# Optimization experiments

Hardware: AMD Instinct MI355X
Metric: run time of the kernel (lower is better)

## Reference

```python
import jax, jax.numpy as jnp
import numpy as np
from jax.ops import segment_sum, segment_max

N_ENT = 50000
N_REL = 200
E = 800000
D = 128      # entity_dim
R = 128      # relation_dim
H = 8        # num_heads
HD = D // H  # head_dim
SLOPE = 0.2  # LeakyReLU negative slope

def leaky(x):
    return jnp.where(x >= 0, x, SLOPE * x)

def setup_inputs() -> dict:
    key = jax.random.key(0)
    ks = jax.random.split(key, 8)
    h = jax.random.normal(ks[0], (N_ENT, D), dtype=jnp.float32)
    z = jax.random.normal(ks[1], (N_REL, R), dtype=jnp.float32)
    # weights stored (in_features, out_features); scaled ~ kaiming-ish
    Wc_w = jax.random.normal(ks[2], (D + R, D), dtype=jnp.float32) / np.sqrt(D + R)
    P_w = jax.random.normal(ks[3], (2 * D + R, D), dtype=jnp.float32) / np.sqrt(2 * D + R)
    y_w = jax.random.normal(ks[4], (D, H), dtype=jnp.float32) / np.sqrt(D)
    residual_weight = jnp.ones((1,), dtype=jnp.float32)
    edge_index = jax.random.randint(ks[5], (2, E), 0, N_ENT, dtype=jnp.int32)
    edge_type = jax.random.randint(ks[6], (E,), 0, N_REL, dtype=jnp.int32)
    return {"h": h, "z": z, "Wc_w": Wc_w, "P_w": P_w, "y_w": y_w,
            "residual_weight": residual_weight,
            "edge_index": edge_index, "edge_type": edge_type}

def reference(h, z, Wc_w, P_w, y_w, residual_weight, edge_index, edge_type):
    src, dst = edge_index[0], edge_index[1]
    n = h.shape[0]
    # per-destination degree and mean relation embedding z_bar_i
    deg = segment_sum(jnp.ones_like(dst, dtype=h.dtype), dst, num_segments=n)  # (N,)
    z_edge = z[edge_type]                                                      # (E,R)
    z_bar = segment_sum(z_edge, dst, num_segments=n) / jnp.maximum(deg, 1.0)[:, None]  # (N,R)
    # split P_hat over the concat [h_i || h_j || z_k]
    P1, P2, P3 = P_w[:D], P_w[D:2 * D], P_w[2 * D:]
    hP1 = h @ P1   # (N,D) dst part
    hP2 = h @ P2   # (N,D) src part
    zP3 = z @ P3   # (N_REL,D)
    pre_edge = hP1[dst] + hP2[src] + zP3[edge_type]      # (E,D)
    attn_e = leaky(pre_edge) @ y_w                        # (E,H)
    pre_self = hP1 + hP2 + z_bar @ P3                     # (N,D)  b_self=[h_i,h_i,z_bar]
    attn_s = leaky(pre_self) @ y_w                        # (N,H)
    # segment softmax over {self} U incoming edges, per head
    m_e = segment_max(attn_e, dst, num_segments=n)        # -inf for empty segments
    m = jnp.maximum(attn_s, m_e)                          # (N,H)
    e_e = jnp.exp(attn_e - m[dst])                        # (E,H)
    e_s = jnp.exp(attn_s - m)                             # (N,H)
    denom = segment_sum(e_e, dst, num_segments=n) + e_s   # (N,H)
    w_e = e_e / denom[dst]                                # (E,H)
    w_s = e_s / denom                                     # (N,H)
    # Wc over concats [h || z]
    Wc_h, Wc_z = Wc_w[:D], Wc_w[D:]
    hWc = h @ Wc_h                                        # (N,D)
    zWc = z @ Wc_z                                        # (N_REL,D)
    t_e = hWc[src] + zWc[edge_type]                       # (E,D)
    t_s = hWc + z_bar @ Wc_z                              # (N,D)
    # per-head weighted sum
    agg_e = segment_sum(w_e[:, :, None] * t_e.reshape(-1, H, HD), dst, num_segments=n)
    agg = agg_e + w_s[:, :, None] * t_s.reshape(-1, H, HD)  # (N,H,HD)
    h_new = leaky(agg.reshape(-1, D) + residual_weight * h)
    # nodes without incoming edges keep their original representation
    return jnp.where(deg[:, None] > 0, h_new, h)
```

## Files before the change

### kernel.cpp

```cpp
#include <hip/hip_runtime.h>

#define NE 50000
#define NR 200
#define EE 800000
#define DD 128
#define HH 8
#define SLOTS 64
#define SLOPE 0.2f

__device__ __forceinline__ float leaky(float x){ return x >= 0.f ? x : SLOPE*x; }

__device__ __forceinline__ float head_reduce(float4 pa, float4 pb, int hh){
  bool b0 = (hh & 1) != 0;
  bool b1 = (hh & 2) != 0;
  bool b2 = (hh & 4) != 0;
  float q0 = (b0 ? pa.y : pa.x) + __shfl_xor(b0 ? pa.x : pa.y, 1, 64);
  float q1 = (b0 ? pa.w : pa.z) + __shfl_xor(b0 ? pa.z : pa.w, 1, 64);
  float q2 = (b0 ? pb.y : pb.x) + __shfl_xor(b0 ? pb.x : pb.y, 1, 64);
  float q3 = (b0 ? pb.w : pb.z) + __shfl_xor(b0 ? pb.z : pb.w, 1, 64);
  float r0 = (b1 ? q1 : q0) + __shfl_xor(b1 ? q0 : q1, 2, 64);
  float r1 = (b1 ? q3 : q2) + __shfl_xor(b1 ? q2 : q3, 2, 64);
  float a  = (b2 ? r1 : r0) + __shfl_xor(b2 ? r0 : r1, 4, 64);
  a += __shfl_xor(a, 8, 64);
  a += __shfl_xor(a, 16, 64);
  a += __shfl_xor(a, 32, 64);
  return a;
}

__global__ void k_zero(int* __restrict__ cnt){
  int i = blockIdx.x*256 + threadIdx.x;
  if (i < NE) cnt[i] = 0;
}

__global__ void k_scatter(const int* __restrict__ edge_index,
                          const int* __restrict__ edge_type,
                          int* __restrict__ cnt, int* __restrict__ slot){
  int e = blockIdx.x*256 + threadIdx.x;
  if (e >= EE) return;
  int s = edge_index[e];
  int d = edge_index[EE + e];
  int t = edge_type[e];
  int pos = atomicAdd(&cnt[d], 1);
  if (pos < SLOTS) slot[d*SLOTS + pos] = s | (t << 16);
}

__global__ void k_zsmall(const float* __restrict__ z, const float* __restrict__ P_w,
                         const float* __restrict__ Wc_w,
                         float* __restrict__ zP3, float* __restrict__ zWc){
  int r = blockIdx.x, c = threadIdx.x;
  float a1 = 0.f, a2 = 0.f;
  for (int d = 0; d < DD; d++){
    float zv = z[r*DD + d];
    a1 = fmaf(zv, P_w[(2*DD + d)*DD + c], a1);
    a2 = fmaf(zv, Wc_w[(DD + d)*DD + c], a2);
  }
  zP3[r*DD + c] = a1;
  zWc[r*DD + c] = a2;
}

__global__ __launch_bounds__(256) void k_hgemm(const float* __restrict__ h,
    const float* __restrict__ P_w, const float* __restrict__ Wc_w,
    float* __restrict__ hP1, float* __restrict__ hP2, float* __restrict__ hWc){
  __shared__ float hs[64][DD + 4];
  int tid = threadIdx.x;
  int row0 = blockIdx.x * 64;
  for (int f = tid; f < 64*DD/4; f += 256){
    int r = f >> 5, c4 = f & 31;
    int gr = row0 + r;
    float4 v = (gr < NE) ? ((const float4*)(h + (size_t)gr*DD))[c4]
                         : make_float4(0.f,0.f,0.f,0.f);
    hs[r][c4*4+0] = v.x; hs[r][c4*4+1] = v.y;
    hs[r][c4*4+2] = v.z; hs[r][c4*4+3] = v.w;
  }
  __syncthreads();
  int r0 = (tid >> 4) * 4, c0 = (tid & 15) * 8;
  #pragma unroll
  for (int mi = 0; mi < 3; mi++){
    const float* W = (mi == 0) ? P_w : (mi == 1) ? (P_w + DD*DD) : Wc_w;
    float*       O = (mi == 0) ? hP1 : (mi == 1) ? hP2 : hWc;
    float acc[4][8];
    #pragma unroll
    for (int i = 0; i < 4; i++)
      #pragma unroll
      for (int j = 0; j < 8; j++) acc[i][j] = 0.f;
    for (int d = 0; d < DD; d++){
      float av[4];
      #pragma unroll
      for (int i = 0; i < 4; i++) av[i] = hs[r0+i][d];
      float4 b0 = *(const float4*)(W + d*DD + c0);
      float4 b1 = *(const float4*)(W + d*DD + c0 + 4);
      float bv[8] = {b0.x,b0.y,b0.z,b0.w,b1.x,b1.y,b1.z,b1.w};
      #pragma unroll
      for (int i = 0; i < 4; i++)
        #pragma unroll
        for (int j = 0; j < 8; j++)
          acc[i][j] = fmaf(av[i], bv[j], acc[i][j]);
    }
    #pragma unroll
    for (int i = 0; i < 4; i++){
      int gr = row0 + r0 + i;
      if (gr < NE){
        *(float4*)(O + (size_t)gr*DD + c0)     = make_float4(acc[i][0],acc[i][1],acc[i][2],acc[i][3]);
        *(float4*)(O + (size_t)gr*DD + c0 + 4) = make_float4(acc[i][4],acc[i][5],acc[i][6],acc[i][7]);
      }
    }
  }
}

__global__ __launch_bounds__(256) void k_node(
    const float* __restrict__ hP1, const float* __restrict__ hP2,
    const float* __restrict__ hWc, const float* __restrict__ zP3,
    const float* __restrict__ zWc, const float* __restrict__ h,
    const float* __restrict__ y_w, const float* __restrict__ rw_p,
    const int* __restrict__ cnt, const int* __restrict__ slot,
    float* __restrict__ out){
  int lane = threadIdx.x & 63;
  int n = blockIdx.x*4 + (threadIdx.x >> 6);
  if (n >= NE) return;
  int hh  = lane & 7;
  int sub = lane >> 3;
  int di  = hh*8 + sub;
  int deg = cnt[n]; if (deg > SLOTS) deg = SLOTS;
  float2 hn = ((const float2*)(h + (size_t)n*DD))[di];
  if (deg == 0){ ((float2*)(out + (size_t)n*DD))[di] = hn; return; }
  float2 p1  = ((const float2*)(hP1 + (size_t)n*DD))[di];
  float2 p2n = ((const float2*)(hP2 + (size_t)n*DD))[di];
  float2 wcn = ((const float2*)(hWc + (size_t)n*DD))[di];
  int d0 = di*2;
  const float4* y4 = (const float4*)(y_w + (size_t)d0*HH);
  float4 A = y4[0], B = y4[1], C = y4[2], Dv = y4[3];
  int my_slot = 0;
  if (lane < deg) my_slot = slot[(size_t)n*SLOTS + lane];
  float m_h = -1e30f, den = 0.f;
  float aggx = 0.f, aggy = 0.f;
  float sP3x = 0.f, sP3y = 0.f, sWcx = 0.f, sWcy = 0.f;
  for (int j = 0; j < deg; j++){
    int v = __shfl(my_slot, j, 64);
    int s = v & 0xFFFF;
    int t = v >> 16;
    float2 a2 = ((const float2*)(hP2 + (size_t)s*DD))[di];
    float2 b2 = ((const float2*)(zP3 + (size_t)t*DD))[di];
    float2 c2 = ((const float2*)(hWc + (size_t)s*DD))[di];
    float2 e2 = ((const float2*)(zWc + (size_t)t*DD))[di];
    sP3x += b2.x; sP3y += b2.y;
    sWcx += e2.x; sWcy += e2.y;
    float l0 = leaky(p1.x + a2.x + b2.x);
    float l1 = leaky(p1.y + a2.y + b2.y);
    float4 pa, pb;
    pa.x = l0*A.x + l1*C.x;  pa.y = l0*A.y + l1*C.y;
    pa.z = l0*A.z + l1*C.z;  pa.w = l0*A.w + l1*C.w;
    pb.x = l0*B.x + l1*Dv.x; pb.y = l0*B.y + l1*Dv.y;
    pb.z = l0*B.z + l1*Dv.z; pb.w = l0*B.w + l1*Dv.w;
    float attn = head_reduce(pa, pb, hh);
    float nm = fmaxf(m_h, attn);
    float sc = __expf(m_h - nm);
    float w  = __expf(attn - nm);
    den = den*sc + w;
    m_h = nm;
    float tx = c2.x + e2.x, ty = c2.y + e2.y;
    aggx = aggx*sc + w*tx;
    aggy = aggy*sc + w*ty;
  }
  float invdeg = 1.f/(float)deg;
  float l0 = leaky(p1.x + p2n.x + sP3x*invdeg);
  float l1 = leaky(p1.y + p2n.y + sP3y*invdeg);
  float4 pa, pb;
  pa.x = l0*A.x + l1*C.x;  pa.y = l0*A.y + l1*C.y;
  pa.z = l0*A.z + l1*C.z;  pa.w = l0*A.w + l1*C.w;
  pb.x = l0*B.x + l1*Dv.x; pb.y = l0*B.y + l1*Dv.y;
  pb.z = l0*B.z + l1*Dv.z; pb.w = l0*B.w + l1*Dv.w;
  float attnS = head_reduce(pa, pb, hh);
  float nm = fmaxf(m_h, attnS);
  float sc = __expf(m_h - nm);
  float w  = __expf(attnS - nm);
  den = den*sc + w;
  float tx = wcn.x + sWcx*invdeg, ty = wcn.y + sWcy*invdeg;
  aggx = aggx*sc + w*tx;
  aggy = aggy*sc + w*ty;
  float rw = rw_p[0];
  float inv_den = 1.f/den;
  float o0 = leaky(aggx*inv_den + rw*hn.x);
  float o1 = leaky(aggy*inv_den + rw*hn.y);
  ((float2*)(out + (size_t)n*DD))[di] = make_float2(o0, o1);
}

extern "C" void kernel_launch(void* const* d_in, const int* in_sizes, int n_in,
                              void* d_out, int out_size, void* d_ws, size_t ws_size,
                              hipStream_t stream){
  const float* h    = (const float*)d_in[0];
  const float* z    = (const float*)d_in[1];
  const float* Wc_w = (const float*)d_in[2];
  const float* P_w  = (const float*)d_in[3];
  const float* y_w  = (const float*)d_in[4];
  const float* rw   = (const float*)d_in[5];
  const int* edge_index = (const int*)d_in[6];
  const int* edge_type  = (const int*)d_in[7];
  float* out = (float*)d_out;

  char* ws = (char*)d_ws;
  float* hP1 = (float*)ws;  ws += (size_t)NE*DD*4;
  float* hP2 = (float*)ws;  ws += (size_t)NE*DD*4;
  float* hWc = (float*)ws;  ws += (size_t)NE*DD*4;
  float* zP3 = (float*)ws;  ws += (size_t)NR*DD*4;
  float* zWc = (float*)ws;  ws += (size_t)NR*DD*4;
  int*   cnt = (int*)ws;    ws += (size_t)NE*4;
  int*   slot= (int*)ws;    ws += (size_t)NE*SLOTS*4;

  hipLaunchKernelGGL(k_zero,    dim3((NE+255)/256), dim3(256), 0, stream, cnt);
  hipLaunchKernelGGL(k_scatter, dim3((EE+255)/256), dim3(256), 0, stream,
                     edge_index, edge_type, cnt, slot);
  hipLaunchKernelGGL(k_zsmall,  dim3(NR), dim3(DD), 0, stream, z, P_w, Wc_w, zP3, zWc);
  hipLaunchKernelGGL(k_hgemm,   dim3((NE+63)/64), dim3(256), 0, stream,
                     h, P_w, Wc_w, hP1, hP2, hWc);
  hipLaunchKernelGGL(k_node,    dim3((NE+3)/4), dim3(256), 0, stream,
                     hP1, hP2, hWc, zP3, zWc, h, y_w, rw, cnt, slot, out);
}
```

Measured before the change: 485.5 us.

## Interleave per-source projections and batch edge gathers four at a time

Stores hP2 and hWc interleaved in a single row (and zP3/zWc likewise), so each edge gather reads one contiguous 1KB row instead of two separate rows. The node kernel's edge loop is unrolled by four, issuing all gathers before the attention math to raise memory-level parallelism, and it uses readlane for the slot broadcast. The GEMM reads shared memory as float4 along the k dimension. The cost is more registers in the node kernel, which may reduce occupancy.

Measured after the change: 452.9 us. -6.7%, faster.

```diff
diff --git a/kernel.cpp b/kernel.cpp
--- a/kernel.cpp
+++ b/kernel.cpp
@@ -27,6 +27,29 @@
   return a;
 }
 
+__device__ __forceinline__ float edge_attn(float2 p1, float2 a, float2 b,
+    float4 A, float4 B, float4 C, float4 Dv, int hh){
+  float l0 = leaky(p1.x + a.x + b.x);
+  float l1 = leaky(p1.y + a.y + b.y);
+  float4 pa, pb;
+  pa.x = l0*A.x + l1*C.x;  pa.y = l0*A.y + l1*C.y;
+  pa.z = l0*A.z + l1*C.z;  pa.w = l0*A.w + l1*C.w;
+  pb.x = l0*B.x + l1*Dv.x; pb.y = l0*B.y + l1*Dv.y;
+  pb.z = l0*B.z + l1*Dv.z; pb.w = l0*B.w + l1*Dv.w;
+  return head_reduce(pa, pb, hh);
+}
+
+__device__ __forceinline__ void sm_update(float attn, float tx, float ty,
+    float& m_h, float& den, float& aggx, float& aggy){
+  float nm = fmaxf(m_h, attn);
+  float sc = __expf(m_h - nm);
+  float w  = __expf(attn - nm);
+  den = den*sc + w;
+  m_h = nm;
+  aggx = aggx*sc + w*tx;
+  aggy = aggy*sc + w*ty;
+}
+
 __global__ void k_zero(int* __restrict__ cnt){
   int i = blockIdx.x*256 + threadIdx.x;
   if (i < NE) cnt[i] = 0;
@@ -45,8 +68,7 @@
 }
 
 __global__ void k_zsmall(const float* __restrict__ z, const float* __restrict__ P_w,
-                         const float* __restrict__ Wc_w,
-                         float* __restrict__ zP3, float* __restrict__ zWc){
+                         const float* __restrict__ Wc_w, float* __restrict__ zPW){
   int r = blockIdx.x, c = threadIdx.x;
   float a1 = 0.f, a2 = 0.f;
   for (int d = 0; d < DD; d++){
@@ -54,13 +76,13 @@
     a1 = fmaf(zv, P_w[(2*DD + d)*DD + c], a1);
     a2 = fmaf(zv, Wc_w[(DD + d)*DD + c], a2);
   }
-  zP3[r*DD + c] = a1;
-  zWc[r*DD + c] = a2;
+  zPW[(size_t)r*(2*DD) + c]      = a1;
+  zPW[(size_t)r*(2*DD) + DD + c] = a2;
 }
 
 __global__ __launch_bounds__(256) void k_hgemm(const float* __restrict__ h,
     const float* __restrict__ P_w, const float* __restrict__ Wc_w,
-    float* __restrict__ hP1, float* __restrict__ hP2, float* __restrict__ hWc){
+    float* __restrict__ hP1, float* __restrict__ hPW){
   __shared__ float hs[64][DD + 4];
   int tid = threadIdx.x;
   int row0 = blockIdx.x * 64;
@@ -77,40 +99,46 @@
   #pragma unroll
   for (int mi = 0; mi < 3; mi++){
     const float* W = (mi == 0) ? P_w : (mi == 1) ? (P_w + DD*DD) : Wc_w;
-    float*       O = (mi == 0) ? hP1 : (mi == 1) ? hP2 : hWc;
     float acc[4][8];
     #pragma unroll
     for (int i = 0; i < 4; i++)
       #pragma unroll
       for (int j = 0; j < 8; j++) acc[i][j] = 0.f;
-    for (int d = 0; d < DD; d++){
-      float av[4];
-      #pragma unroll
-      for (int i = 0; i < 4; i++) av[i] = hs[r0+i][d];
-      float4 b0 = *(const float4*)(W + d*DD + c0);
-      float4 b1 = *(const float4*)(W + d*DD + c0 + 4);
-      float bv[8] = {b0.x,b0.y,b0.z,b0.w,b1.x,b1.y,b1.z,b1.w};
+    for (int d4 = 0; d4 < DD/4; d4++){
+      float avs[4][4];
       #pragma unroll
       for (int i = 0; i < 4; i++)
+        *(float4*)&avs[i][0] = *(const float4*)&hs[r0+i][d4*4];
+      #pragma unroll
+      for (int dd = 0; dd < 4; dd++){
+        int d = d4*4 + dd;
+        float4 b0 = *(const float4*)(W + d*DD + c0);
+        float4 b1 = *(const float4*)(W + d*DD + c0 + 4);
+        float bv[8] = {b0.x,b0.y,b0.z,b0.w,b1.x,b1.y,b1.z,b1.w};
         #pragma unroll
-        for (int j = 0; j < 8; j++)
-          acc[i][j] = fmaf(av[i], bv[j], acc[i][j]);
+        for (int i = 0; i < 4; i++)
+          #pragma unroll
+          for (int j = 0; j < 8; j++)
+            acc[i][j] = fmaf(avs[i][dd], bv[j], acc[i][j]);
+      }
     }
     #pragma unroll
     for (int i = 0; i < 4; i++){
       int gr = row0 + r0 + i;
       if (gr < NE){
-        *(float4*)(O + (size_t)gr*DD + c0)     = make_float4(acc[i][0],acc[i][1],acc[i][2],acc[i][3]);
-        *(float4*)(O + (size_t)gr*DD + c0 + 4) = make_float4(acc[i][4],acc[i][5],acc[i][6],acc[i][7]);
+        float* O = (mi == 0) ? (hP1 + (size_t)gr*DD + c0)
+                 : (mi == 1) ? (hPW + (size_t)gr*(2*DD) + c0)
+                             : (hPW + (size_t)gr*(2*DD) + DD + c0);
+        *(float4*)(O)     = make_float4(acc[i][0],acc[i][1],acc[i][2],acc[i][3]);
+        *(float4*)(O + 4) = make_float4(acc[i][4],acc[i][5],acc[i][6],acc[i][7]);
       }
     }
   }
 }
 
 __global__ __launch_bounds__(256) void k_node(
-    const float* __restrict__ hP1, const float* __restrict__ hP2,
-    const float* __restrict__ hWc, const float* __restrict__ zP3,
-    const float* __restrict__ zWc, const float* __restrict__ h,
+    const float* __restrict__ hP1, const float* __restrict__ hPW,
+    const float* __restrict__ zPW, const float* __restrict__ h,
     const float* __restrict__ y_w, const float* __restrict__ rw_p,
     const int* __restrict__ cnt, const int* __restrict__ slot,
     float* __restrict__ out){
@@ -120,13 +148,14 @@
   int hh  = lane & 7;
   int sub = lane >> 3;
   int di  = hh*8 + sub;
+  int d0  = di*2;
   int deg = cnt[n]; if (deg > SLOTS) deg = SLOTS;
   float2 hn = ((const float2*)(h + (size_t)n*DD))[di];
   if (deg == 0){ ((float2*)(out + (size_t)n*DD))[di] = hn; return; }
   float2 p1  = ((const float2*)(hP1 + (size_t)n*DD))[di];
-  float2 p2n = ((const float2*)(hP2 + (size_t)n*DD))[di];
-  float2 wcn = ((const float2*)(hWc + (size_t)n*DD))[di];
-  int d0 = di*2;
+  const float* rowN = hPW + (size_t)n*(2*DD);
+  float2 p2n = *(const float2*)(rowN + d0);
+  float2 wcn = *(const float2*)(rowN + DD + d0);
   const float4* y4 = (const float4*)(y_w + (size_t)d0*HH);
   float4 A = y4[0], B = y4[1], C = y4[2], Dv = y4[3];
   int my_slot = 0;
@@ -134,42 +163,46 @@
   float m_h = -1e30f, den = 0.f;
   float aggx = 0.f, aggy = 0.f;
   float sP3x = 0.f, sP3y = 0.f, sWcx = 0.f, sWcy = 0.f;
-  for (int j = 0; j < deg; j++){
-    int v = __shfl(my_slot, j, 64);
-    int s = v & 0xFFFF;
-    int t = v >> 16;
-    float2 a2 = ((const float2*)(hP2 + (size_t)s*DD))[di];
-    float2 b2 = ((const float2*)(zP3 + (size_t)t*DD))[di];
-    float2 c2 = ((const float2*)(hWc + (size_t)s*DD))[di];
-    float2 e2 = ((const float2*)(zWc + (size_t)t*DD))[di];
+  int j = 0;
+  for (; j + 4 <= deg; j += 4){
+    float2 av[4], bv[4], cv[4], ev[4];
+    #pragma unroll
+    for (int k = 0; k < 4; k++){
+      int v = __builtin_amdgcn_readlane(my_slot, j + k);
+      const float* rp = hPW + (size_t)(v & 0xFFFF)*(2*DD);
+      const float* zp = zPW + (size_t)((unsigned)v >> 16)*(2*DD);
+      av[k] = *(const float2*)(rp + d0);
+      cv[k] = *(const float2*)(rp + DD + d0);
+      bv[k] = *(const float2*)(zp + d0);
+      ev[k] = *(const float2*)(zp + DD + d0);
+    }
+    float at[4];
+    #pragma unroll
+    for (int k = 0; k < 4; k++){
+      sP3x += bv[k].x; sP3y += bv[k].y;
+      sWcx += ev[k].x; sWcy += ev[k].y;
+      at[k] = edge_attn(p1, av[k], bv[k], A, B, C, Dv, hh);
+    }
+    #pragma unroll
+    for (int k = 0; k < 4; k++)
+      sm_update(at[k], cv[k].x + ev[k].x, cv[k].y + ev[k].y, m_h, den, aggx, aggy);
+  }
+  for (; j < deg; j++){
+    int v = __builtin_amdgcn_readlane(my_slot, j);
+    const float* rp = hPW + (size_t)(v & 0xFFFF)*(2*DD);
+    const float* zp = zPW + (size_t)((unsigned)v >> 16)*(2*DD);
+    float2 a2 = *(const float2*)(rp + d0);
+    float2 c2 = *(const float2*)(rp + DD + d0);
+    float2 b2 = *(const float2*)(zp + d0);
+    float2 e2 = *(const float2*)(zp + DD + d0);
     sP3x += b2.x; sP3y += b2.y;
     sWcx += e2.x; sWcy += e2.y;
-    float l0 = leaky(p1.x + a2.x + b2.x);
-    float l1 = leaky(p1.y + a2.y + b2.y);
-    float4 pa, pb;
-    pa.x = l0*A.x + l1*C.x;  pa.y = l0*A.y + l1*C.y;
-    pa.z = l0*A.z + l1*C.z;  pa.w = l0*A.w + l1*C.w;
-    pb.x = l0*B.x + l1*Dv.x; pb.y = l0*B.y + l1*Dv.y;
-    pb.z = l0*B.z + l1*Dv.z; pb.w = l0*B.w + l1*Dv.w;
-    float attn = head_reduce(pa, pb, hh);
-    float nm = fmaxf(m_h, attn);
-    float sc = __expf(m_h - nm);
-    float w  = __expf(attn - nm);
-    den = den*sc + w;
-    m_h = nm;
-    float tx = c2.x + e2.x, ty = c2.y + e2.y;
-    aggx = aggx*sc + w*tx;
-    aggy = aggy*sc + w*ty;
+    float at = edge_attn(p1, a2, b2, A, B, C, Dv, hh);
+    sm_update(at, c2.x + e2.x, c2.y + e2.y, m_h, den, aggx, aggy);
   }
   float invdeg = 1.f/(float)deg;
-  float l0 = leaky(p1.x + p2n.x + sP3x*invdeg);
-  float l1 = leaky(p1.y + p2n.y + sP3y*invdeg);
-  float4 pa, pb;
-  pa.x = l0*A.x + l1*C.x;  pa.y = l0*A.y + l1*C.y;
-  pa.z = l0*A.z + l1*C.z;  pa.w = l0*A.w + l1*C.w;
-  pb.x = l0*B.x + l1*Dv.x; pb.y = l0*B.y + l1*Dv.y;
-  pb.z = l0*B.z + l1*Dv.z; pb.w = l0*B.w + l1*Dv.w;
-  float attnS = head_reduce(pa, pb, hh);
+  float2 zb1 = make_float2(sP3x*invdeg, sP3y*invdeg);
+  float attnS = edge_attn(p1, p2n, zb1, A, B, C, Dv, hh);
   float nm = fmaxf(m_h, attnS);
   float sc = __expf(m_h - nm);
   float w  = __expf(attnS - nm);
@@ -199,19 +232,17 @@
 
   char* ws = (char*)d_ws;
   float* hP1 = (float*)ws;  ws += (size_t)NE*DD*4;
-  float* hP2 = (float*)ws;  ws += (size_t)NE*DD*4;
-  float* hWc = (float*)ws;  ws += (size_t)NE*DD*4;
-  float* zP3 = (float*)ws;  ws += (size_t)NR*DD*4;
-  float* zWc = (float*)ws;  ws += (size_t)NR*DD*4;
+  float* hPW = (float*)ws;  ws += (size_t)NE*2*DD*4;
+  float* zPW = (float*)ws;  ws += (size_t)NR*2*DD*4;
   int*   cnt = (int*)ws;    ws += (size_t)NE*4;
   int*   slot= (int*)ws;    ws += (size_t)NE*SLOTS*4;
 
   hipLaunchKernelGGL(k_zero,    dim3((NE+255)/256), dim3(256), 0, stream, cnt);
   hipLaunchKernelGGL(k_scatter, dim3((EE+255)/256), dim3(256), 0, stream,
                      edge_index, edge_type, cnt, slot);
-  hipLaunchKernelGGL(k_zsmall,  dim3(NR), dim3(DD), 0, stream, z, P_w, Wc_w, zP3, zWc);
+  hipLaunchKernelGGL(k_zsmall,  dim3(NR), dim3(DD), 0, stream, z, P_w, Wc_w, zPW);
   hipLaunchKernelGGL(k_hgemm,   dim3((NE+63)/64), dim3(256), 0, stream,
-                     h, P_w, Wc_w, hP1, hP2, hWc);
+                     h, P_w, Wc_w, hP1, hPW);
   hipLaunchKernelGGL(k_node,    dim3((NE+3)/4), dim3(256), 0, stream,
-                     hP1, hP2, hWc, zP3, zWc, h, y_w, rw, cnt, slot, out);
-}
+                     hP1, hPW, zPW, h, y_w, rw, cnt, slot, out);
+}
```
